# Performance work log

Hardware: AMD Instinct MI355X
Metric: run time of the kernel (lower is better)

Reference implementation:

```python
import jax, jax.numpy as jnp
import numpy as np

B, S, H, D = 4, 4096, 8, 128
EPS = 1e-6


def layernorm(x, g, b, axes):
    m = jnp.mean(x, axis=axes, keepdims=True)
    v = jnp.mean(jnp.square(x - m), axis=axes, keepdims=True)
    return (x - m) / jnp.sqrt(v + EPS) * g + b


def setup_inputs() -> dict:
    key = jax.random.key(0)
    ks = jax.random.split(key, 6)
    scale = 0.05
    return {
        "heads_input": jax.random.normal(ks[0], (B, S, H, D), jnp.float32),
        # GroupLinear trans_hid: per-head (2D -> 3D)
        "W_hid": jax.random.normal(ks[1], (H, 2 * D, 3 * D), jnp.float32) * scale,
        "b_hid": jax.random.normal(ks[2], (H, 3 * D), jnp.float32) * scale,
        # GroupLinear trans_og: per-head (2D -> D)
        "W_og": jax.random.normal(ks[3], (H, 2 * D, D), jnp.float32) * scale,
        "b_og": jax.random.normal(ks[4], (H, D), jnp.float32) * scale,
        # LayerNorm affine params (elementwise_affine=True)
        "ln_csum_g": jnp.ones((H, D), jnp.float32),
        "ln_csum_b": jnp.zeros((H, D), jnp.float32),
        "ln_hid_g": jnp.ones((H, 3, D), jnp.float32),
        "ln_hid_b": jnp.zeros((H, 3, D), jnp.float32),
        "ln_og_g": jnp.ones((H, D), jnp.float32),
        "ln_og_b": jnp.zeros((H, D), jnp.float32),
        "init_cx": jnp.zeros((1, H, D), jnp.float32),
    }


def reference(heads_input, W_hid, b_hid, W_og, b_og, ln_csum_g, ln_csum_b,
              ln_hid_g, ln_hid_b, ln_og_g, ln_og_b, init_cx):
    b, s, h, d = heads_input.shape
    # shifted cumulative sum over time, then LayerNorm over (head, dim)
    shifted = jnp.concatenate(
        [jnp.zeros((b, 1, h, d), heads_input.dtype), heads_input[:, :-1]], axis=1)
    csum = layernorm(jnp.cumsum(shifted, axis=1), ln_csum_g, ln_csum_b, (-2, -1))
    cat = jnp.concatenate([heads_input, csum], axis=-1)        # [b,s,h,2d]
    hid = jnp.einsum('bshi,hio->bsho', cat, W_hid) + b_hid     # [b,s,h,3d]
    hid = layernorm(hid.reshape(b, s, h, 3, d), ln_hid_g, ln_hid_b, (-3, -2, -1))
    igate, fgate, hidden = hid[..., 0, :], hid[..., 1, :], hid[..., 2, :]
    fgate = jax.nn.sigmoid(fgate)
    igh = jax.nn.sigmoid(igate) * jax.nn.relu(hidden)
    # LGateFunc: cell_t = fgate_t * cell_{t-1} + igh_t, cell_0 = init_cx
    c0 = jnp.broadcast_to(init_cx, (b, h, d)).astype(heads_input.dtype)
    def step(c, fi):
        f, i = fi
        c = f * c + i
        return c, c
    _, cells = jax.lax.scan(step, c0,
                            (fgate.transpose(1, 0, 2, 3), igh.transpose(1, 0, 2, 3)))
    cell = cells.transpose(1, 0, 2, 3)                          # [b,s,h,d]
    og_in = jnp.concatenate([heads_input, cell], axis=-1)       # [b,s,h,2d]
    og = layernorm(jnp.einsum('bshi,hio->bsho', og_in, W_og) + b_og,
                   ln_og_g, ln_og_b, (-2, -1))
    return jax.nn.sigmoid(og) * cell
```

## Files before the change

kernel.cpp:

```cpp
#include <hip/hip_runtime.h>

#define EPSF 1e-6f


typedef __attribute__((ext_vector_type(8))) short short8v;
typedef __attribute__((ext_vector_type(4))) float float4v;

__device__ __forceinline__ float sigm(float x) { return 1.0f / (1.0f + __expf(-x)); }

__device__ __forceinline__ unsigned short f2bf(float f) {
    unsigned int u = __float_as_uint(f);
    u = (u + 0x7fffu + ((u >> 16) & 1u)) >> 16;
    return (unsigned short)u;
}
__device__ __forceinline__ float bf2f(unsigned short s) { return __uint_as_float(((unsigned int)s) << 16); }
__device__ __forceinline__ float bf2f_lo(unsigned int p) { return __uint_as_float(p << 16); }
__device__ __forceinline__ float bf2f_hi(unsigned int p) { return __uint_as_float(p & 0xffff0000u); }
__device__ __forceinline__ unsigned int pack2bf(float a, float b) {
    return (unsigned int)f2bf(a) | ((unsigned int)f2bf(b) << 16);
}

__device__ __forceinline__ void block_reduce2(float& a, float& b) {
#pragma unroll
    for (int off = 32; off > 0; off >>= 1) {
        a += __shfl_down(a, off);
        b += __shfl_down(b, off);
    }
    __shared__ float sa[8], sb[8];
    int wid = threadIdx.x >> 6;
    int lane = threadIdx.x & 63;
    if (lane == 0) { sa[wid] = a; sb[wid] = b; }
    __syncthreads();
    a = sa[0] + sa[1] + sa[2] + sa[3];
    b = sb[0] + sb[1] + sb[2] + sb[3];
}

__global__ __launch_bounds__(256) void k_prep_w(const float* __restrict__ W, unsigned short* __restrict__ Wt,
                                                int Nw) {
    int idx = blockIdx.x * 256 + threadIdx.x;
    int k = idx & 255;
    int rest = idx >> 8;
    int o = rest % Nw;
    int h = rest / Nw;
    Wt[idx] = f2bf(W[((size_t)h * 256 + k) * Nw + o]);
}

__global__ __launch_bounds__(256) void k_cumsum_a(const float* __restrict__ X, float* __restrict__ cS,
                                                  unsigned short* __restrict__ XB) {
    int t = blockIdx.x * 256 + threadIdx.x;
    int d = t & 127, h = (t >> 7) & 7, k = (t >> 10) & 63, b = t >> 16;
    size_t xbase = (((size_t)(b * 4096 + k * 64)) * 8 + h) * 128 + d;
    size_t pbase = ((size_t)h * 16384 + b * 4096 + k * 64) * 128 + d;
    float s = 0.f;
    for (int j = 0; j < 64; ++j) {
        unsigned short xb = f2bf(X[xbase + (size_t)j * 1024]);
        XB[pbase + (size_t)j * 128] = xb;
        s += bf2f(xb);
    }
    cS[(size_t)((b * 8 + h) * 128 + d) * 64 + k] = s;
}

__global__ __launch_bounds__(256) void k_cumsum_b(const float* __restrict__ cS, float* __restrict__ cO) {
    int wave = (blockIdx.x * 256 + threadIdx.x) >> 6;
    int lane = threadIdx.x & 63;
    size_t idx = (size_t)wave * 64 + lane;
    float v = cS[idx];
    float incl = v;
#pragma unroll
    for (int d = 1; d < 64; d <<= 1) {
        float t = __shfl_up(incl, d);
        if (lane >= d) incl += t;
    }
    cO[idx] = incl - v;
}

__global__ __launch_bounds__(256) void k_cumsum_c(const unsigned short* __restrict__ XB,
                                                  const float* __restrict__ cO,
                                                  unsigned short* __restrict__ CSUMB) {
    int t = blockIdx.x * 256 + threadIdx.x;
    int d = t & 127, h = (t >> 7) & 7, k = (t >> 10) & 63, b = t >> 16;
    int ch = (b * 8 + h) * 128 + d;
    float run = cO[(size_t)ch * 64 + k];
    size_t pbase = ((size_t)h * 16384 + b * 4096 + k * 64) * 128 + d;
    for (int j = 0; j < 64; ++j) {
        float x = bf2f(XB[pbase + (size_t)j * 128]);
        CSUMB[pbase + (size_t)j * 128] = f2bf(run);
        run += x;
    }
}

__global__ __launch_bounds__(256) void k_ln_csum(const unsigned short* __restrict__ CSUMB,
                                                 unsigned short* __restrict__ CSB,
                                                 const float* __restrict__ g, const float* __restrict__ bb) {
    int bs = blockIdx.x, t = threadIdx.x;
    int h = t >> 5, c = t & 31;
    size_t u2i = ((size_t)h * 16384 + bs) * 32 + c;
    uint2 u = ((const uint2*)CSUMB)[u2i];
    float4 v;
    v.x = bf2f_lo(u.x); v.y = bf2f_hi(u.x);
    v.z = bf2f_lo(u.y); v.w = bf2f_hi(u.y);
    float s = v.x + v.y + v.z + v.w;
    float ss = v.x * v.x + v.y * v.y + v.z * v.z + v.w * v.w;
    block_reduce2(s, ss);
    float m = s * (1.f / 1024.f);
    float var = ss * (1.f / 1024.f) - m * m;
    float r = rsqrtf(fmaxf(var, 0.f) + EPSF);
    float4 gv = ((const float4*)g)[t];
    float4 bv = ((const float4*)bb)[t];
    uint2 o;
    o.x = pack2bf((v.x - m) * r * gv.x + bv.x, (v.y - m) * r * gv.y + bv.y);
    o.y = pack2bf((v.z - m) * r * gv.z + bv.z, (v.w - m) * r * gv.w + bv.w);
    ((uint2*)CSB)[u2i] = o;
}

__global__ __launch_bounds__(512) void k_gemm_bf16(const unsigned short* __restrict__ A1,
                                                   const unsigned short* __restrict__ A2,
                                                   const unsigned short* __restrict__ Wt,
                                                   const float* __restrict__ bias,
                                                   unsigned short* __restrict__ OUT, int Nw, int m0,
                                                   int nbx) {
    __shared__ short As[4][8192];
    __shared__ short Bs[4][8192];
    int bid = blockIdx.x;
    int h = bid & 7;
    int rest = bid >> 3;
    int bx = rest % nbx;
    int by = rest / nbx;
    int t0 = threadIdx.x;
    int lane = t0 & 63, wid = t0 >> 6;
    int wr = wid >> 1, wc = wid & 1;
    int l15 = lane & 15, l4 = lane >> 4;
    int lr = lane >> 3, lc = lane & 7;
    const int bxc = bx * 128;
    const size_t mbase = (size_t)(m0 + by * 128);
    const size_t aplane = (size_t)h * 16384;

    float4v acc[2][4];
#pragma unroll
    for (int i = 0; i < 2; ++i)
#pragma unroll
        for (int j = 0; j < 4; ++j) acc[i][j] = (float4v)(0.f);

    auto STAGE = [&](int t) {
        const unsigned short* src = (t < 2) ? A1 : A2;
        int kofs = (t & 1) * 64;
#pragma unroll
        for (int it = 0; it < 2; ++it) {
            int r0 = wid * 16 + it * 8;
            int r = r0 + lr;
            int c = lc ^ (r & 7);
            size_t g = (aplane + mbase + r) * 128 + kofs + c * 8;
            __builtin_amdgcn_global_load_lds((const __attribute__((address_space(1))) void*)(src + g),
                                             (__attribute__((address_space(3))) void*)(&As[t][r0 * 64]),
                                             16, 0, 0);
        }
#pragma unroll
        for (int it = 0; it < 2; ++it) {
            int n0 = wid * 16 + it * 8;
            int cl = n0 + lr;
            int c = lc ^ (cl & 7);
            size_t g = ((size_t)(h * Nw + bxc + cl)) * 256 + t * 64 + c * 8;
            __builtin_amdgcn_global_load_lds((const __attribute__((address_space(1))) void*)(Wt + g),
                                             (__attribute__((address_space(3))) void*)(&Bs[t][n0 * 64]),
                                             16, 0, 0);
        }
    };

    STAGE(0); STAGE(1); STAGE(2); STAGE(3);

#pragma unroll
    for (int t = 0; t < 4; ++t) {
        if (t == 0)      asm volatile("s_waitcnt vmcnt(12)" ::: "memory");
        else if (t == 1) asm volatile("s_waitcnt vmcnt(8)" ::: "memory");
        else if (t == 2) asm volatile("s_waitcnt vmcnt(4)" ::: "memory");
        else             asm volatile("s_waitcnt vmcnt(0)" ::: "memory");
        __builtin_amdgcn_s_barrier();
        __builtin_amdgcn_sched_barrier(0);
#pragma unroll
        for (int kk = 0; kk < 2; ++kk) {
            short8v a[2], b[4];
#pragma unroll
            for (int i = 0; i < 2; ++i) {
                int r = wr * 32 + i * 16 + l15;
                int slot = (kk * 4 + l4) ^ (r & 7);
                a[i] = *(const short8v*)(&As[t][r * 64 + slot * 8]);
            }
#pragma unroll
            for (int j = 0; j < 4; ++j) {
                int c = wc * 64 + j * 16 + l15;
                int slot = (kk * 4 + l4) ^ (c & 7);
                b[j] = *(const short8v*)(&Bs[t][c * 64 + slot * 8]);
            }
#pragma unroll
            for (int i = 0; i < 2; ++i)
#pragma unroll
                for (int j = 0; j < 4; ++j)
                    acc[i][j] = __builtin_amdgcn_mfma_f32_16x16x32_bf16(a[i], b[j], acc[i][j], 0, 0, 0);
        }
    }
#pragma unroll
    for (int j = 0; j < 4; ++j) {
        int o = bxc + wc * 64 + j * 16 + l15;
        float bv = bias[h * Nw + o];
#pragma unroll
        for (int i = 0; i < 2; ++i) {
            int mlb = by * 128 + wr * 32 + i * 16 + l4 * 4;
#pragma unroll
            for (int q = 0; q < 4; ++q) {
                OUT[((size_t)(mlb + q) * 8 + h) * Nw + o] = f2bf(acc[i][j][q] + bv);
            }
        }
    }
}

__global__ __launch_bounds__(256) void k_ln_gates(const unsigned short* __restrict__ HID,
                                                  unsigned short* __restrict__ FG,
                                                  unsigned short* __restrict__ IG,
                                                  const float* __restrict__ g, const float* __restrict__ bb,
                                                  int m0) {
    __shared__ float sm[3072];
    int bsl = blockIdx.x, t = threadIdx.x;
    int bs = m0 + bsl;
    const uint4* row = (const uint4*)(HID + (size_t)bsl * 3072);
    float s = 0.f, ss = 0.f;
    for (int idx = t; idx < 384; idx += 256) {
        uint4 u = row[idx];
        float f0 = bf2f_lo(u.x), f1 = bf2f_hi(u.x);
        float f2 = bf2f_lo(u.y), f3 = bf2f_hi(u.y);
        float f4 = bf2f_lo(u.z), f5 = bf2f_hi(u.z);
        float f6 = bf2f_lo(u.w), f7 = bf2f_hi(u.w);
        float* p = sm + idx * 8;
        p[0] = f0; p[1] = f1; p[2] = f2; p[3] = f3; p[4] = f4; p[5] = f5; p[6] = f6; p[7] = f7;
        s += f0 + f1 + f2 + f3 + f4 + f5 + f6 + f7;
        ss += f0 * f0 + f1 * f1 + f2 * f2 + f3 * f3 + f4 * f4 + f5 * f5 + f6 * f6 + f7 * f7;
    }
    block_reduce2(s, ss);
    float m = s * (1.f / 3072.f);
    float var = ss * (1.f / 3072.f) - m * m;
    float r = rsqrtf(fmaxf(var, 0.f) + EPSF);
    int u0 = t * 4;
    int h = u0 >> 7;
    int d0 = u0 & 127;
    float fr[4], ir[4];
#pragma unroll
    for (int q = 0; q < 4; ++q) {
        int d = d0 + q;
        float yi = sm[h * 384 + d];
        float yf = sm[h * 384 + 128 + d];
        float yh = sm[h * 384 + 256 + d];
        float ni = (yi - m) * r * g[(h * 3 + 0) * 128 + d] + bb[(h * 3 + 0) * 128 + d];
        float nf = (yf - m) * r * g[(h * 3 + 1) * 128 + d] + bb[(h * 3 + 1) * 128 + d];
        float nh = (yh - m) * r * g[(h * 3 + 2) * 128 + d] + bb[(h * 3 + 2) * 128 + d];
        fr[q] = sigm(nf);
        ir[q] = sigm(ni) * fmaxf(nh, 0.f);
    }
    uint2 fo, io;
    fo.x = pack2bf(fr[0], fr[1]); fo.y = pack2bf(fr[2], fr[3]);
    io.x = pack2bf(ir[0], ir[1]); io.y = pack2bf(ir[2], ir[3]);
    ((uint2*)(FG + (size_t)bs * 1024))[t] = fo;
    ((uint2*)(IG + (size_t)bs * 1024))[t] = io;
}

__global__ __launch_bounds__(256) void k_scan_a(const unsigned short* __restrict__ FG,
                                                const unsigned short* __restrict__ IG,
                                                float* __restrict__ cF, float* __restrict__ cC) {
    int t = blockIdx.x * 256 + threadIdx.x;
    int d2 = t & 63, h = (t >> 6) & 7, k = (t >> 9) & 63, b = t >> 15;
    size_t base = (((size_t)(b * 4096 + k * 64)) * 8 + h) * 64 + d2;
    const unsigned int* FGu = (const unsigned int*)FG;
    const unsigned int* IGu = (const unsigned int*)IG;
    float F0 = 1.f, C0 = 0.f, F1 = 1.f, C1 = 0.f;
    for (int j = 0; j < 64; ++j) {
        unsigned int fg = FGu[base + (size_t)j * 512];
        unsigned int ig = IGu[base + (size_t)j * 512];
        float f0 = bf2f_lo(fg), f1 = bf2f_hi(fg);
        C0 = fmaf(f0, C0, bf2f_lo(ig)); F0 *= f0;
        C1 = fmaf(f1, C1, bf2f_hi(ig)); F1 *= f1;
    }
    size_t ci0 = ((size_t)((b * 8 + h) * 128 + d2 * 2)) * 64 + k;
    cF[ci0] = F0; cC[ci0] = C0;
    cF[ci0 + 64] = F1; cC[ci0 + 64] = C1;
}

__global__ __launch_bounds__(256) void k_scan_b(const float* __restrict__ cF, const float* __restrict__ cC,
                                                const float* __restrict__ initcx, float* __restrict__ cI) {
    int wave = (blockIdx.x * 256 + threadIdx.x) >> 6;
    int lane = threadIdx.x & 63;
    size_t idx = (size_t)wave * 64 + lane;
    float F = cF[idx], C = cC[idx];
#pragma unroll
    for (int d = 1; d < 64; d <<= 1) {
        float Fp = __shfl_up(F, d);
        float Cp = __shfl_up(C, d);
        if (lane >= d) { C = fmaf(Cp, F, C); F *= Fp; }
    }
    float Fe = __shfl_up(F, 1);
    float Ce = __shfl_up(C, 1);
    if (lane == 0) { Fe = 1.f; Ce = 0.f; }
    float c0 = initcx[wave & 1023];
    cI[idx] = fmaf(Fe, c0, Ce);
}

__global__ __launch_bounds__(256) void k_scan_c(const unsigned short* __restrict__ FG,
                                                const unsigned short* __restrict__ IG,
                                                unsigned short* __restrict__ CLB,
                                                const float* __restrict__ cI) {
    int t = blockIdx.x * 256 + threadIdx.x;
    int d2 = t & 63, h = (t >> 6) & 7, k = (t >> 9) & 63, b = t >> 15;
    size_t base = (((size_t)(b * 4096 + k * 64)) * 8 + h) * 64 + d2;
    size_t pbase = ((size_t)h * 16384 + b * 4096 + k * 64) * 64 + d2;
    const unsigned int* FGu = (const unsigned int*)FG;
    const unsigned int* IGu = (const unsigned int*)IG;
    unsigned int* CLu = (unsigned int*)CLB;
    size_t ci0 = ((size_t)((b * 8 + h) * 128 + d2 * 2)) * 64 + k;
    float c0 = cI[ci0], c1 = cI[ci0 + 64];
    for (int j = 0; j < 64; ++j) {
        unsigned int fg = FGu[base + (size_t)j * 512];
        unsigned int ig = IGu[base + (size_t)j * 512];
        c0 = fmaf(bf2f_lo(fg), c0, bf2f_lo(ig));
        c1 = fmaf(bf2f_hi(fg), c1, bf2f_hi(ig));
        CLu[pbase + (size_t)j * 64] = pack2bf(c0, c1);
    }
}

__global__ __launch_bounds__(256) void k_ln_out(const unsigned short* __restrict__ OG,
                                                const unsigned short* __restrict__ CLB,
                                                const float* __restrict__ g, const float* __restrict__ bb,
                                                float* __restrict__ OUT, int m0) {
    int bsl = blockIdx.x, t = threadIdx.x;
    int bs = m0 + bsl;
    uint2 u = ((const uint2*)(OG + (size_t)bsl * 1024))[t];
    float4 v;
    v.x = bf2f_lo(u.x); v.y = bf2f_hi(u.x);
    v.z = bf2f_lo(u.y); v.w = bf2f_hi(u.y);
    float s = v.x + v.y + v.z + v.w;
    float ss = v.x * v.x + v.y * v.y + v.z * v.z + v.w * v.w;
    block_reduce2(s, ss);
    float m = s * (1.f / 1024.f);
    float var = ss * (1.f / 1024.f) - m * m;
    float r = rsqrtf(fmaxf(var, 0.f) + EPSF);
    float4 gv = ((const float4*)g)[t];
    float4 bv = ((const float4*)bb)[t];
    int h = t >> 5, c = t & 31;
    uint2 cu = ((const uint2*)CLB)[((size_t)h * 16384 + bs) * 32 + c];
    float4 cv;
    cv.x = bf2f_lo(cu.x); cv.y = bf2f_hi(cu.x);
    cv.z = bf2f_lo(cu.y); cv.w = bf2f_hi(cu.y);
    float4 o;
    o.x = sigm((v.x - m) * r * gv.x + bv.x) * cv.x;
    o.y = sigm((v.y - m) * r * gv.y + bv.y) * cv.y;
    o.z = sigm((v.z - m) * r * gv.z + bv.z) * cv.z;
    o.w = sigm((v.w - m) * r * gv.w + bv.w) * cv.w;
    ((float4*)(OUT + (size_t)bs * 1024))[t] = o;
}

extern "C" void kernel_launch(void* const* d_in, const int* in_sizes, int n_in,
                              void* d_out, int out_size, void* d_ws, size_t ws_size,
                              hipStream_t stream) {
    const float* X      = (const float*)d_in[0];
    const float* W_hid  = (const float*)d_in[1];
    const float* b_hid  = (const float*)d_in[2];
    const float* W_og   = (const float*)d_in[3];
    const float* b_og   = (const float*)d_in[4];
    const float* g_cs   = (const float*)d_in[5];
    const float* b_cs   = (const float*)d_in[6];
    const float* g_hid  = (const float*)d_in[7];
    const float* b_hidl = (const float*)d_in[8];
    const float* g_og   = (const float*)d_in[9];
    const float* b_ogl  = (const float*)d_in[10];
    const float* initcx = (const float*)d_in[11];

    float* ws = (float*)d_ws;
    const size_t O_SC    = 0ull;
    const size_t O_XB    = 1310720ull;
    const size_t O_CSUMB = 9699328ull;
    const size_t O_CSB   = 18087936ull;
    const size_t O_IGB   = 26476544ull;
    const size_t O_CLB   = 34865152ull;
    const size_t O_WTH   = 43253760ull;
    const size_t O_WTO   = 43646976ull;
    const size_t O_HID   = 43778048ull;

    float* cS = ws + O_SC;
    float* cO = cS + 262144;
    float* cF = cO + 262144;
    float* cC = cF + 262144;
    float* cI = cC + 262144;
    unsigned short* XB    = (unsigned short*)(ws + O_XB);
    unsigned short* CSUMB = (unsigned short*)(ws + O_CSUMB);
    unsigned short* FGB   = CSUMB;
    unsigned short* CSB   = (unsigned short*)(ws + O_CSB);
    unsigned short* IGB   = (unsigned short*)(ws + O_IGB);
    unsigned short* CLB   = (unsigned short*)(ws + O_CLB);
    unsigned short* WTH   = (unsigned short*)(ws + O_WTH);
    unsigned short* WTO   = (unsigned short*)(ws + O_WTO);
    unsigned short* HIDC  = (unsigned short*)(ws + O_HID);

    size_t avail = (ws_size / 4 > O_HID) ? ws_size / 4 - O_HID : 0;
    int CH = 1024;
    for (int c = 16384; c >= 1024; c >>= 1) {
        if ((size_t)c * 1536ull <= avail) { CH = c; break; }
    }
    const int NC = 16384 / CH;

    dim3 blk(256);
    dim3 blkg(512);
    k_prep_w<<<3072, blk, 0, stream>>>(W_hid, WTH, 384);
    k_prep_w<<<1024, blk, 0, stream>>>(W_og, WTO, 128);
    k_cumsum_a<<<1024, blk, 0, stream>>>(X, cS, XB);
    k_cumsum_b<<<1024, blk, 0, stream>>>(cS, cO);
    k_cumsum_c<<<1024, blk, 0, stream>>>(XB, cO, CSUMB);
    k_ln_csum<<<16384, blk, 0, stream>>>(CSUMB, CSB, g_cs, b_cs);
    for (int c = 0; c < NC; ++c) {
        int m0 = c * CH;
        k_gemm_bf16<<<8 * 3 * (CH / 128), blkg, 0, stream>>>(XB, CSB, WTH, b_hid, HIDC, 384, m0, 3);
        k_ln_gates<<<CH, blk, 0, stream>>>(HIDC, FGB, IGB, g_hid, b_hidl, m0);
    }
    k_scan_a<<<512, blk, 0, stream>>>(FGB, IGB, cF, cC);
    k_scan_b<<<1024, blk, 0, stream>>>(cF, cC, initcx, cI);
    k_scan_c<<<512, blk, 0, stream>>>(FGB, IGB, CLB, cI);
    for (int c = 0; c < NC; ++c) {
        int m0 = c * CH;
        k_gemm_bf16<<<8 * 1 * (CH / 128), blkg, 0, stream>>>(XB, CLB, WTO, b_og, HIDC, 128, m0, 1);
        k_ln_out<<<CH, blk, 0, stream>>>(HIDC, CLB, g_og, b_ogl, (float*)d_out, m0);
    }
}
```

Baseline: 254.4 us.

## Stage GEMM output tile through LDS for coalesced stores; merge weight prep kernels

Result: slower. 279.4 us (+9.8%).

```diff
diff --git a/kernel.cpp b/kernel.cpp
--- a/kernel.cpp
+++ b/kernel.cpp
@@ -35,14 +35,24 @@
     b = sb[0] + sb[1] + sb[2] + sb[3];
 }
 
-__global__ __launch_bounds__(256) void k_prep_w(const float* __restrict__ W, unsigned short* __restrict__ Wt,
-                                                int Nw) {
+__global__ __launch_bounds__(256) void k_prep_w(const float* __restrict__ Wh, const float* __restrict__ Wo,
+                                                unsigned short* __restrict__ WTH,
+                                                unsigned short* __restrict__ WTO) {
     int idx = blockIdx.x * 256 + threadIdx.x;
-    int k = idx & 255;
-    int rest = idx >> 8;
-    int o = rest % Nw;
-    int h = rest / Nw;
-    Wt[idx] = f2bf(W[((size_t)h * 256 + k) * Nw + o]);
+    if (idx < 786432) {
+        int k = idx & 255;
+        int rest = idx >> 8;
+        int o = rest % 384;
+        int h = rest / 384;
+        WTH[idx] = f2bf(Wh[((size_t)h * 256 + k) * 384 + o]);
+    } else {
+        int i2 = idx - 786432;
+        int k = i2 & 255;
+        int rest = i2 >> 8;
+        int o = rest & 127;
+        int h = rest >> 7;
+        WTO[i2] = f2bf(Wo[((size_t)h * 256 + k) * 128 + o]);
+    }
 }
 
 __global__ __launch_bounds__(256) void k_cumsum_a(const float* __restrict__ X, float* __restrict__ cS,
@@ -198,18 +208,32 @@
                     acc[i][j] = __builtin_amdgcn_mfma_f32_16x16x32_bf16(a[i], b[j], acc[i][j], 0, 0, 0);
         }
     }
+
+    __syncthreads();
+    short* Cs = &As[0][0];
 #pragma unroll
     for (int j = 0; j < 4; ++j) {
-        int o = bxc + wc * 64 + j * 16 + l15;
-        float bv = bias[h * Nw + o];
+        int col = wc * 64 + j * 16 + l15;
+        float bv = bias[h * Nw + bxc + col];
 #pragma unroll
         for (int i = 0; i < 2; ++i) {
-            int mlb = by * 128 + wr * 32 + i * 16 + l4 * 4;
+            int rbase = wr * 32 + i * 16 + l4 * 4;
 #pragma unroll
             for (int q = 0; q < 4; ++q) {
-                OUT[((size_t)(mlb + q) * 8 + h) * Nw + o] = f2bf(acc[i][j][q] + bv);
+                Cs[(rbase + q) * 136 + col] = f2bf(acc[i][j][q] + bv);
             }
         }
+    }
+    __syncthreads();
+    {
+        int row = t0 >> 2, seg = t0 & 3;
+        const uint4* src = (const uint4*)(Cs + row * 136 + seg * 32);
+        size_t gb = ((size_t)(by * 128 + row) * 8 + h) * Nw + bxc + seg * 32;
+        uint4 v0 = src[0], v1 = src[1], v2 = src[2], v3 = src[3];
+        *(uint4*)(&OUT[gb]) = v0;
+        *(uint4*)(&OUT[gb + 8]) = v1;
+        *(uint4*)(&OUT[gb + 16]) = v2;
+        *(uint4*)(&OUT[gb + 24]) = v3;
     }
 }
 
@@ -405,8 +429,7 @@
 
     dim3 blk(256);
     dim3 blkg(512);
-    k_prep_w<<<3072, blk, 0, stream>>>(W_hid, WTH, 384);
-    k_prep_w<<<1024, blk, 0, stream>>>(W_og, WTO, 128);
+    k_prep_w<<<4096, blk, 0, stream>>>(W_hid, W_og, WTH, WTO);
     k_cumsum_a<<<1024, blk, 0, stream>>>(X, cS, XB);
     k_cumsum_b<<<1024, blk, 0, stream>>>(cS, cO);
     k_cumsum_c<<<1024, blk, 0, stream>>>(XB, cO, CSUMB);
```
